# Performance work log

Measured on AMD Instinct MI355X. Metric: run time of the kernel, lower is better.

Reference implementation:

```python
import jax, jax.numpy as jnp
import numpy as np

B, S, E, H = 8, 1024, 1024, 16
D = E // H


def setup_inputs() -> dict:
    key = jax.random.key(0)
    ks = jax.random.split(key, 5)
    s = 1.0 / np.sqrt(E)
    return {
        "hidden_states": jax.random.normal(ks[0], (B, S, E), dtype=jnp.float32),
        "w_q": jax.random.normal(ks[1], (E, E), dtype=jnp.float32) * s,
        "w_k": jax.random.normal(ks[2], (E, E), dtype=jnp.float32) * s,
        "w_v": jax.random.normal(ks[3], (E, E), dtype=jnp.float32) * s,
        "w_out": jax.random.normal(ks[4], (E, E), dtype=jnp.float32) * s,
        "b_out": jnp.zeros((E,), dtype=jnp.float32),
    }


def reference(hidden_states, w_q, w_k, w_v, w_out, b_out):
    b, s = hidden_states.shape[0], hidden_states.shape[1]
    # Linear projections (weights stored as [in, out] = torch W^T)
    q = hidden_states @ w_q
    k = hidden_states @ w_k
    v = hidden_states @ w_v
    # Faithful to the original: raw reshape (B,S,E)->(B,H,S,D), NOT a head-split transpose
    q = q.reshape(b, H, s, D)
    k = k.reshape(b, H, s, D)
    v = v.reshape(b, H, s, D)
    # Scores scaled by embedding_size**-0.5 (original quirk, not head_dim**-0.5)
    scores = jnp.einsum("bhsd,bhtd->bhst", q, k) * (E ** -0.5)
    attn = jax.nn.softmax(scores, axis=-1)
    out = jnp.einsum("bhst,bhtd->bhsd", attn, v)  # [B,H,S,D]
    out = out.transpose(0, 2, 1, 3).reshape(b, s, E)  # [B,S,E]
    return out @ w_out + b_out
```

## Files before the change

### kernel.cpp

```cpp
#include <hip/hip_runtime.h>
#include <hip/hip_bf16.h>
#include <stdint.h>
#include <stddef.h>

static constexpr int Bb = 8, Ss = 1024, Ee = 1024, Hh = 16, Dd = 64;
static constexpr int Mm = Bb * Ss;

typedef __attribute__((ext_vector_type(8))) short frag8;
typedef __attribute__((ext_vector_type(4))) float fx4;
typedef __attribute__((ext_vector_type(4))) short s4v;

#define GP(p) ((const __attribute__((address_space(1))) void*)(p))
#define LP(p) ((__attribute__((address_space(3))) void*)(p))

static constexpr float QSC = 0.045084220027780106f;

__device__ inline short f2bf(float x) {
  union { float f; unsigned u; } c; c.f = x;
  unsigned u = c.u;
  unsigned r = (u + 0x7FFFu + ((u >> 16) & 1u)) >> 16;
  return (short)r;
}

__global__ __launch_bounds__(256) void cvt_kernel(const float* __restrict__ in,
                                                  short* __restrict__ out, int n4) {
  int i = blockIdx.x * 256 + threadIdx.x;
  if (i >= n4) return;
  float4 v = *((const float4*)in + i);
  union { short s[4]; uint2 u; } o;
  o.s[0] = f2bf(v.x); o.s[1] = f2bf(v.y); o.s[2] = f2bf(v.z); o.s[3] = f2bf(v.w);
  *(uint2*)(out + (size_t)i * 4) = o.u;
}

__global__ __launch_bounds__(256) void transpose_cvt4(const float* __restrict__ w0,
                                                      const float* __restrict__ w1,
                                                      const float* __restrict__ w2,
                                                      const float* __restrict__ w3,
                                                      short* __restrict__ WtBase) {
  __shared__ short tile[32][33];
  const int z = blockIdx.z;
  const float* W = z == 0 ? w0 : (z == 1 ? w1 : (z == 2 ? w2 : w3));
  short* Wt = WtBase + (size_t)z * 1024 * 1024;
  const int bx = blockIdx.x * 32;
  const int by = blockIdx.y * 32;
  const int tx = threadIdx.x & 31, ty = threadIdx.x >> 5;
  #pragma unroll
  for (int j = 0; j < 32; j += 8)
    tile[ty + j][tx] = f2bf(W[(size_t)(by + ty + j) * 1024 + bx + tx]);
  __syncthreads();
  #pragma unroll
  for (int j = 0; j < 32; j += 8)
    Wt[(size_t)(bx + ty + j) * 1024 + by + tx] = tile[tx][ty + j];
}

__global__ __launch_bounds__(256) void transpose_v(const short* __restrict__ V,
                                                   short* __restrict__ Vt) {
  __shared__ short tile[64][65];
  const int bh = blockIdx.y;
  const int s0 = blockIdx.x * 64;
  const short* Vb = V + (size_t)bh * 65536;
  short* Vtb = Vt + (size_t)bh * 65536;
  const int tx = threadIdx.x & 63, ty = threadIdx.x >> 6;
  #pragma unroll
  for (int j = 0; j < 64; j += 4)
    tile[ty + j][tx] = Vb[(size_t)(s0 + ty + j) * 64 + tx];
  __syncthreads();
  #pragma unroll
  for (int j = 0; j < 64; j += 4)
    Vtb[(size_t)(ty + j) * 1024 + s0 + tx] = tile[tx][ty + j];
}

__global__ __launch_bounds__(512, 2) void gemm_qkv_8ph(const short* __restrict__ A,
                                                       const short* __restrict__ Bt,
                                                       short* __restrict__ Cq,
                                                       short* __restrict__ Ck,
                                                       short* __restrict__ Cv) {
  __shared__ short As[2][16384];
  __shared__ short Bs[2][16384];
  const int t = threadIdx.x;
  const int w = t >> 6, lane = t & 63;
  const int fm = lane & 15, quad = lane >> 4;
  const int wm = w >> 1, wn = w & 1;
  const int wg = (blockIdx.x & 7) * 48 + (blockIdx.x >> 3);
  const int nt_i = wg % 12, mt_i = wg / 12;
  const int m0 = mt_i * 256, n0 = nt_i * 256;

  int goffA[4], goffB[4];
  #pragma unroll
  for (int i = 0; i < 4; ++i) {
    int c = i * 512 + t, row = c >> 3, col8 = (c & 7) ^ (row & 7);
    goffA[i] = row * 1024 + col8 * 8;
  }
  {
    int row32 = (t >> 3) & 31, hv = t >> 8, col8 = (t & 7) ^ (row32 & 7);
    #pragma unroll
    for (int j = 0; j < 4; ++j)
      goffB[j] = (hv * 128 + j * 32 + row32) * 1024 + col8 * 8;
  }
  const short* Ag = A + (size_t)m0 * 1024;
  const short* Bg = Bt + (size_t)n0 * 1024;

  fx4 acc[4][8];
  #pragma unroll
  for (int i = 0; i < 4; ++i)
    #pragma unroll
    for (int j = 0; j < 8; ++j) acc[i][j] = (fx4){0.f, 0.f, 0.f, 0.f};

  const int s0o = ((0 * 4 + quad) ^ (fm & 7)) * 8;
  const int s1o = ((1 * 4 + quad) ^ (fm & 7)) * 8;
  const int aBase = (wm * 64 + fm) * 64;
  const int bBase = wn * 2048 + fm * 64;

#define STG_A(i, koff, dstbuf) \
  __builtin_amdgcn_global_load_lds(GP(Ag + (koff) + goffA[i]), \
                                   LP((dstbuf) + ((i) * 512 + t) * 8), 16, 0, 0)
#define STG_B(j, koff, dstbuf) \
  __builtin_amdgcn_global_load_lds(GP(Bg + (koff) + goffB[j]), \
                                   LP((dstbuf) + ((j) * 512 + t) * 8), 16, 0, 0)
#define LOAD_B(p) \
  { const short* bp = Bb + (p) * 4096 + bBase; \
    bf[0][0] = *(const frag8*)(bp + s0o); \
    bf[0][1] = *(const frag8*)(bp + s1o); \
    bf[1][0] = *(const frag8*)(bp + 1024 + s0o); \
    bf[1][1] = *(const frag8*)(bp + 1024 + s1o); }
#define MFMA_PH(p) \
  __builtin_amdgcn_s_barrier(); \
  asm volatile("s_waitcnt lgkmcnt(0)" ::: "memory"); \
  __builtin_amdgcn_s_setprio(1); \
  _Pragma("unroll") \
  for (int mf = 0; mf < 4; ++mf) { \
    acc[mf][2*(p)]   = __builtin_amdgcn_mfma_f32_16x16x32_bf16(af[mf][0], bf[0][0], acc[mf][2*(p)],   0, 0, 0); \
    acc[mf][2*(p)]   = __builtin_amdgcn_mfma_f32_16x16x32_bf16(af[mf][1], bf[0][1], acc[mf][2*(p)],   0, 0, 0); \
    acc[mf][2*(p)+1] = __builtin_amdgcn_mfma_f32_16x16x32_bf16(af[mf][0], bf[1][0], acc[mf][2*(p)+1], 0, 0, 0); \
    acc[mf][2*(p)+1] = __builtin_amdgcn_mfma_f32_16x16x32_bf16(af[mf][1], bf[1][1], acc[mf][2*(p)+1], 0, 0, 0); \
  } \
  __builtin_amdgcn_s_setprio(0);

  #pragma unroll
  for (int i = 0; i < 4; ++i) STG_A(i, 0, &As[0][0]);
  #pragma unroll
  for (int j = 0; j < 4; ++j) STG_B(j, 0, &Bs[0][0]);
  asm volatile("s_waitcnt vmcnt(0)" ::: "memory");
  __builtin_amdgcn_s_barrier();

  for (int kt = 0; kt < 16; ++kt) {
    const short* Ab = As[kt & 1];
    const short* Bb = Bs[kt & 1];
    short* An = (short*)As[(kt & 1) ^ 1];
    short* Bn = (short*)Bs[(kt & 1) ^ 1];
    const int kn = (kt + 1) * 64;
    const bool pf = kt < 15;
    frag8 af[4][2], bf[2][2];

    #pragma unroll
    for (int mf = 0; mf < 4; ++mf) {
      const short* ap = Ab + aBase + mf * 1024;
      af[mf][0] = *(const frag8*)(ap + s0o);
      af[mf][1] = *(const frag8*)(ap + s1o);
    }
    LOAD_B(0);
    if (pf) {
      STG_A(0, kn, An); STG_A(1, kn, An); STG_A(2, kn, An); STG_A(3, kn, An);
      STG_B(0, kn, Bn); STG_B(1, kn, Bn); STG_B(2, kn, Bn); STG_B(3, kn, Bn);
    }
    MFMA_PH(0);
    __builtin_amdgcn_s_barrier();

    LOAD_B(1);
    MFMA_PH(1);
    __builtin_amdgcn_s_barrier();

    LOAD_B(2);
    MFMA_PH(2);
    __builtin_amdgcn_s_barrier();

    LOAD_B(3);
    MFMA_PH(3);
    if (pf) {
      asm volatile("s_waitcnt vmcnt(0)" ::: "memory");
      __builtin_amdgcn_s_barrier();
    }
  }
#undef STG_A
#undef STG_B
#undef LOAD_B
#undef MFMA_PH

  const int nb = n0 >> 10;
  short* dst = nb == 0 ? Cq : (nb == 1 ? Ck : Cv);
  const float scl = (nb == 0) ? QSC : 1.0f;
  const int nl0 = (n0 & 1023) + wn * 128;
  const int rbase = m0 + wm * 64 + quad * 4;
  #pragma unroll
  for (int mf = 0; mf < 4; ++mf)
    #pragma unroll
    for (int nf = 0; nf < 8; ++nf)
      #pragma unroll
      for (int r = 0; r < 4; ++r) {
        int row = rbase + mf * 16 + r;
        int col = nl0 + nf * 16 + fm;
        dst[(size_t)row * 1024 + col] = f2bf(acc[mf][nf][r] * scl);
      }
}

template <int MODE>
__global__ __launch_bounds__(256) void gemm_bt(const short* __restrict__ A,
                                               const short* __restrict__ Bt,
                                               void* __restrict__ C0,
                                               void* __restrict__ C1,
                                               void* __restrict__ C2,
                                               const float* __restrict__ bias,
                                               int M, int N, int K) {
  __shared__ short As[128 * 32];
  __shared__ short Bs[128 * 32];
  const int t = threadIdx.x;
  const int w = t >> 6, lane = t & 63;
  const int fm = lane & 15, quad = lane >> 4;
  const int m0 = blockIdx.y * 128, n0 = blockIdx.x * 128;
  const int wm = (w >> 1) * 64, wn = (w & 1) * 64;
  fx4 acc[4][4];
  #pragma unroll
  for (int i = 0; i < 4; ++i)
    #pragma unroll
    for (int j = 0; j < 4; ++j) acc[i][j] = (fx4){0.f, 0.f, 0.f, 0.f};

  for (int k0 = 0; k0 < K; k0 += 32) {
    #pragma unroll
    for (int i = 0; i < 2; ++i) {
      int chunk = i * 256 + t;
      int row = chunk >> 2, cc = chunk & 3;
      __builtin_amdgcn_global_load_lds(GP(A + (size_t)(m0 + row) * K + k0 + cc * 8),
                                       LP(As + chunk * 8), 16, 0, 0);
      __builtin_amdgcn_global_load_lds(GP(Bt + (size_t)(n0 + row) * K + k0 + cc * 8),
                                       LP(Bs + chunk * 8), 16, 0, 0);
    }
    __syncthreads();
    frag8 af[4], bfr[4];
    #pragma unroll
    for (int mt = 0; mt < 4; ++mt)
      af[mt] = *(const frag8*)(As + (wm + mt * 16 + fm) * 32 + quad * 8);
    #pragma unroll
    for (int nt = 0; nt < 4; ++nt)
      bfr[nt] = *(const frag8*)(Bs + (wn + nt * 16 + fm) * 32 + quad * 8);
    #pragma unroll
    for (int mt = 0; mt < 4; ++mt)
      #pragma unroll
      for (int nt = 0; nt < 4; ++nt)
        acc[mt][nt] = __builtin_amdgcn_mfma_f32_16x16x32_bf16(af[mt], bfr[nt], acc[mt][nt], 0, 0, 0);
    __syncthreads();
  }
  #pragma unroll
  for (int mt = 0; mt < 4; ++mt)
    #pragma unroll
    for (int nt = 0; nt < 4; ++nt)
      #pragma unroll
      for (int r = 0; r < 4; ++r) {
        int row = m0 + wm + mt * 16 + quad * 4 + r;
        int col = n0 + wn + nt * 16 + fm;
        ((float*)C0)[(size_t)row * N + col] = acc[mt][nt][r] + bias[col];
      }
}

__global__ __launch_bounds__(256, 2) void attn_kernel(const short* __restrict__ Q,
                                                      const short* __restrict__ K,
                                                      const short* __restrict__ Vt,
                                                      short* __restrict__ Ctx) {
  __shared__ short Ks[2][4096];
  __shared__ short Vs[2][4096];
  __shared__ short Plds[4 * 64 * 72];
  const int bh = blockIdx.x, qt = blockIdx.y;
  const int t = threadIdx.x;
  const int w = t >> 6, lane = t & 63;
  const int fm = lane & 15, quad = lane >> 4;
  const short* Qb = Q + (size_t)bh * 65536;
  const short* Kb = K + (size_t)bh * 65536;
  const short* Vb = Vt + (size_t)bh * 65536;
  const int q0 = qt * 256 + w * 64;
  short* myP = Plds + w * 4608;

  frag8 qb[4][2];
  #pragma unroll
  for (int g = 0; g < 4; ++g)
    #pragma unroll
    for (int h = 0; h < 2; ++h)
      qb[g][h] = *(const frag8*)(Qb + (size_t)(q0 + g * 16 + fm) * 64 + h * 32 + quad * 8);

  fx4 O[4][4];
  #pragma unroll
  for (int g = 0; g < 4; ++g)
    #pragma unroll
    for (int nt = 0; nt < 4; ++nt) O[g][nt] = (fx4){0.f, 0.f, 0.f, 0.f};
  float lp[4] = {0.f, 0.f, 0.f, 0.f};

  int koff[2], voff[2], loff[2];
  #pragma unroll
  for (int i = 0; i < 2; ++i) {
    int c = i * 256 + t;
    int cf = c & 15, cq = (c >> 4) & 3, ch = (c >> 6) & 1, cg = c >> 7;
    koff[i] = (cg * 16 + cf) * 64 + ch * 32 + cq * 8;
    voff[i] = (cg * 16 + cf) * 1024 + ch * 32 + cq * 8;
    loff[i] = c * 8;
  }

  #pragma unroll
  for (int i = 0; i < 2; ++i) {
    __builtin_amdgcn_global_load_lds(GP(Kb + koff[i]), LP(&Ks[0][0] + loff[i]), 16, 0, 0);
    __builtin_amdgcn_global_load_lds(GP(Vb + voff[i]), LP(&Vs[0][0] + loff[i]), 16, 0, 0);
  }
  __syncthreads();

  for (int c = 0; c < 16; ++c) {
    const int cur = c & 1;
    if (c < 15) {
      const int key0n = (c + 1) * 64;
      #pragma unroll
      for (int i = 0; i < 2; ++i) {
        __builtin_amdgcn_global_load_lds(GP(Kb + (size_t)key0n * 64 + koff[i]),
                                         LP(&Ks[cur ^ 1][0] + loff[i]), 16, 0, 0);
        __builtin_amdgcn_global_load_lds(GP(Vb + (size_t)key0n + voff[i]),
                                         LP(&Vs[cur ^ 1][0] + loff[i]), 16, 0, 0);
      }
    }
    const short* Kc = &Ks[cur][0];
    const short* Vc = &Vs[cur][0];

    #pragma unroll
    for (int s = 0; s < 4; ++s) {
      frag8 k0 = *(const frag8*)(Kc + (s * 2 + 0) * 512 + lane * 8);
      frag8 k1 = *(const frag8*)(Kc + (s * 2 + 1) * 512 + lane * 8);
      #pragma unroll
      for (int g = 0; g < 4; ++g) {
        fx4 z = (fx4){0.f, 0.f, 0.f, 0.f};
        z = __builtin_amdgcn_mfma_f32_16x16x32_bf16(k0, qb[g][0], z, 0, 0, 0);
        z = __builtin_amdgcn_mfma_f32_16x16x32_bf16(k1, qb[g][1], z, 0, 0, 0);
        s4v pv;
        #pragma unroll
        for (int r = 0; r < 4; ++r) {
          float p = __builtin_amdgcn_exp2f(z[r]);
          lp[g] += p;
          union { float f; unsigned u; } cv; cv.f = p;
          pv[r] = (short)(cv.u >> 16);
        }
        *(s4v*)(myP + (g * 16 + fm) * 72 + s * 16 + quad * 4) = pv;
      }
    }
    asm volatile("s_waitcnt lgkmcnt(0)" ::: "memory");
    #pragma unroll
    for (int h = 0; h < 2; ++h) {
      frag8 pf[4];
      #pragma unroll
      for (int g = 0; g < 4; ++g)
        pf[g] = *(const frag8*)(myP + (g * 16 + fm) * 72 + h * 32 + quad * 8);
      #pragma unroll
      for (int nt = 0; nt < 4; ++nt) {
        frag8 vf = *(const frag8*)(Vc + (nt * 2 + h) * 512 + lane * 8);
        #pragma unroll
        for (int g = 0; g < 4; ++g)
          O[g][nt] = __builtin_amdgcn_mfma_f32_16x16x32_bf16(pf[g], vf, O[g][nt], 0, 0, 0);
      }
    }
    __syncthreads();
  }

  float rl[4][4];
  #pragma unroll
  for (int g = 0; g < 4; ++g) {
    float v = lp[g];
    v += __shfl_xor(v, 16, 64);
    v += __shfl_xor(v, 32, 64);
    float inv = 1.f / v;
    #pragma unroll
    for (int r = 0; r < 4; ++r) rl[g][r] = __shfl(inv, quad * 4 + r, 16);
  }
  const int b = bh >> 4, h = bh & 15;
  #pragma unroll
  for (int g = 0; g < 4; ++g)
    #pragma unroll
    for (int nt = 0; nt < 4; ++nt)
      #pragma unroll
      for (int r = 0; r < 4; ++r) {
        int row = b * 1024 + q0 + g * 16 + quad * 4 + r;
        int col = h * 64 + nt * 16 + fm;
        Ctx[(size_t)row * 1024 + col] = f2bf(O[g][nt][r] * rl[g][r]);
      }
}

extern "C" void kernel_launch(void* const* d_in, const int* in_sizes, int n_in,
                              void* d_out, int out_size, void* d_ws, size_t ws_size,
                              hipStream_t stream) {
  const float* hs = (const float*)d_in[0];
  const float* wq = (const float*)d_in[1];
  const float* wk = (const float*)d_in[2];
  const float* wv = (const float*)d_in[3];
  const float* wo = (const float*)d_in[4];
  const float* bo = (const float*)d_in[5];
  float* out = (float*)d_out;

  char* wp = (char*)d_ws;
  const size_t MB16 = (size_t)Mm * Ee * 2;
  const size_t MB2  = (size_t)Ee * Ee * 2;
  short* Xb  = (short*)wp; wp += MB16;
  short* Wqt = (short*)wp; wp += MB2;
  short* Wkt = (short*)wp; wp += MB2;
  short* Wvt = (short*)wp; wp += MB2;
  short* Wot = (short*)wp; wp += MB2;
  short* Qb  = (short*)wp; wp += MB16;
  short* Kb  = (short*)wp; wp += MB16;
  short* Vb  = (short*)wp; wp += MB16;
  short* Vt  = (short*)wp; wp += MB16;
  short* Ctx = (short*)wp; wp += MB16;

  cvt_kernel<<<(Mm * Ee / 4 + 255) / 256, 256, 0, stream>>>(hs, Xb, Mm * Ee / 4);
  transpose_cvt4<<<dim3(32, 32, 4), 256, 0, stream>>>(wq, wk, wv, wo, Wqt);
  gemm_qkv_8ph<<<384, 512, 0, stream>>>(Xb, Wqt, Qb, Kb, Vb);
  transpose_v<<<dim3(16, 128), 256, 0, stream>>>(Vb, Vt);
  attn_kernel<<<dim3(128, 4), 256, 0, stream>>>(Qb, Kb, Vt, Ctx);
  gemm_bt<1><<<dim3(8, 64), 256, 0, stream>>>(Ctx, Wot, out, nullptr, nullptr, bo, Mm, Ee, Ee);
}
```

Measured before the change: 254.4 us.

## Shrink QKV GEMM tile to 128x256 with split-phase async staging

Halves the M tile of the fused QKV GEMM from 256 to 128 rows and rearranges the 8 waves as 2x4, with each wave computing 64x64. This doubles the grid to 768 blocks and halves the A-tile LDS footprint. The per-k-step schedule goes from four compute phases to two, and the next tile's global-to-LDS loads are split across them with partial vmcnt waits instead of a full drain. The intent is better occupancy and wave balance across CUs plus more overlap of loads with MFMA, at the cost of lower arithmetic intensity per block and more redundant B-tile traffic.

After: 251.0 us. No clear change (-1.3%).

```diff
diff --git a/kernel.cpp b/kernel.cpp
--- a/kernel.cpp
+++ b/kernel.cpp
@@ -75,41 +75,42 @@
                                                        short* __restrict__ Cq,
                                                        short* __restrict__ Ck,
                                                        short* __restrict__ Cv) {
-  __shared__ short As[2][16384];
+  __shared__ short As[2][8192];
   __shared__ short Bs[2][16384];
   const int t = threadIdx.x;
   const int w = t >> 6, lane = t & 63;
   const int fm = lane & 15, quad = lane >> 4;
-  const int wm = w >> 1, wn = w & 1;
-  const int wg = (blockIdx.x & 7) * 48 + (blockIdx.x >> 3);
+  const int wm = w >> 2, wn = w & 3;
+  const int wg = (blockIdx.x & 7) * 96 + (blockIdx.x >> 3);
   const int nt_i = wg % 12, mt_i = wg / 12;
-  const int m0 = mt_i * 256, n0 = nt_i * 256;
-
-  int goffA[4], goffB[4];
-  #pragma unroll
-  for (int i = 0; i < 4; ++i) {
+  const int m0 = mt_i * 128, n0 = nt_i * 256;
+
+  int goffA[2], goffB[4];
+  #pragma unroll
+  for (int i = 0; i < 2; ++i) {
     int c = i * 512 + t, row = c >> 3, col8 = (c & 7) ^ (row & 7);
     goffA[i] = row * 1024 + col8 * 8;
   }
-  {
-    int row32 = (t >> 3) & 31, hv = t >> 8, col8 = (t & 7) ^ (row32 & 7);
-    #pragma unroll
-    for (int j = 0; j < 4; ++j)
-      goffB[j] = (hv * 128 + j * 32 + row32) * 1024 + col8 * 8;
+  #pragma unroll
+  for (int j = 0; j < 4; ++j) {
+    int u = j >> 1, i = j & 1;
+    int c = i * 512 + t, r = c >> 3, col8 = (c & 7) ^ (r & 7);
+    int n = (r >> 5) * 64 + u * 32 + (r & 31);
+    goffB[j] = n * 1024 + col8 * 8;
   }
   const short* Ag = A + (size_t)m0 * 1024;
   const short* Bg = Bt + (size_t)n0 * 1024;
 
-  fx4 acc[4][8];
+  fx4 acc[4][4];
   #pragma unroll
   for (int i = 0; i < 4; ++i)
     #pragma unroll
-    for (int j = 0; j < 8; ++j) acc[i][j] = (fx4){0.f, 0.f, 0.f, 0.f};
-
-  const int s0o = ((0 * 4 + quad) ^ (fm & 7)) * 8;
-  const int s1o = ((1 * 4 + quad) ^ (fm & 7)) * 8;
+    for (int j = 0; j < 4; ++j) acc[i][j] = (fx4){0.f, 0.f, 0.f, 0.f};
+
+  const int s0o = (quad ^ (fm & 7)) * 8;
+  const int s1o = ((4 + quad) ^ (fm & 7)) * 8;
   const int aBase = (wm * 64 + fm) * 64;
-  const int bBase = wn * 2048 + fm * 64;
+  const int bBase = (wn * 32 + fm) * 64;
 
 #define STG_A(i, koff, dstbuf) \
   __builtin_amdgcn_global_load_lds(GP(Ag + (koff) + goffA[i]), \
@@ -118,7 +119,7 @@
   __builtin_amdgcn_global_load_lds(GP(Bg + (koff) + goffB[j]), \
                                    LP((dstbuf) + ((j) * 512 + t) * 8), 16, 0, 0)
 #define LOAD_B(p) \
-  { const short* bp = Bb + (p) * 4096 + bBase; \
+  { const short* bp = Bb + (p) * 8192 + bBase; \
     bf[0][0] = *(const frag8*)(bp + s0o); \
     bf[0][1] = *(const frag8*)(bp + s1o); \
     bf[1][0] = *(const frag8*)(bp + 1024 + s0o); \
@@ -136,11 +137,10 @@
   } \
   __builtin_amdgcn_s_setprio(0);
 
-  #pragma unroll
-  for (int i = 0; i < 4; ++i) STG_A(i, 0, &As[0][0]);
-  #pragma unroll
-  for (int j = 0; j < 4; ++j) STG_B(j, 0, &Bs[0][0]);
-  asm volatile("s_waitcnt vmcnt(0)" ::: "memory");
+  STG_A(0, 0, &As[0][0]); STG_A(1, 0, &As[0][0]);
+  STG_B(0, 0, &Bs[0][0]); STG_B(1, 0, &Bs[0][0]);
+  STG_B(2, 0, &Bs[0][0]); STG_B(3, 0, &Bs[0][0]);
+  asm volatile("s_waitcnt vmcnt(2)" ::: "memory");
   __builtin_amdgcn_s_barrier();
 
   for (int kt = 0; kt < 16; ++kt) {
@@ -159,25 +159,17 @@
       af[mf][1] = *(const frag8*)(ap + s1o);
     }
     LOAD_B(0);
+    if (pf) { STG_A(0, kn, An); STG_A(1, kn, An); STG_B(0, kn, Bn); STG_B(1, kn, Bn); }
+    MFMA_PH(0);
+    if (pf) asm volatile("s_waitcnt vmcnt(4)" ::: "memory");
+    else    asm volatile("s_waitcnt vmcnt(0)" ::: "memory");
+    __builtin_amdgcn_s_barrier();
+
+    LOAD_B(1);
+    if (pf) { STG_B(2, kn, Bn); STG_B(3, kn, Bn); }
+    MFMA_PH(1);
     if (pf) {
-      STG_A(0, kn, An); STG_A(1, kn, An); STG_A(2, kn, An); STG_A(3, kn, An);
-      STG_B(0, kn, Bn); STG_B(1, kn, Bn); STG_B(2, kn, Bn); STG_B(3, kn, Bn);
-    }
-    MFMA_PH(0);
-    __builtin_amdgcn_s_barrier();
-
-    LOAD_B(1);
-    MFMA_PH(1);
-    __builtin_amdgcn_s_barrier();
-
-    LOAD_B(2);
-    MFMA_PH(2);
-    __builtin_amdgcn_s_barrier();
-
-    LOAD_B(3);
-    MFMA_PH(3);
-    if (pf) {
-      asm volatile("s_waitcnt vmcnt(0)" ::: "memory");
+      asm volatile("s_waitcnt vmcnt(2)" ::: "memory");
       __builtin_amdgcn_s_barrier();
     }
   }
@@ -189,12 +181,12 @@
   const int nb = n0 >> 10;
   short* dst = nb == 0 ? Cq : (nb == 1 ? Ck : Cv);
   const float scl = (nb == 0) ? QSC : 1.0f;
-  const int nl0 = (n0 & 1023) + wn * 128;
+  const int nl0 = (n0 & 1023) + wn * 64;
   const int rbase = m0 + wm * 64 + quad * 4;
   #pragma unroll
   for (int mf = 0; mf < 4; ++mf)
     #pragma unroll
-    for (int nf = 0; nf < 8; ++nf)
+    for (int nf = 0; nf < 4; ++nf)
       #pragma unroll
       for (int r = 0; r < 4; ++r) {
         int row = rbase + mf * 16 + r;
@@ -412,7 +404,7 @@
 
   cvt_kernel<<<(Mm * Ee / 4 + 255) / 256, 256, 0, stream>>>(hs, Xb, Mm * Ee / 4);
   transpose_cvt4<<<dim3(32, 32, 4), 256, 0, stream>>>(wq, wk, wv, wo, Wqt);
-  gemm_qkv_8ph<<<384, 512, 0, stream>>>(Xb, Wqt, Qb, Kb, Vb);
+  gemm_qkv_8ph<<<768, 512, 0, stream>>>(Xb, Wqt, Qb, Kb, Vb);
   transpose_v<<<dim3(16, 128), 256, 0, stream>>>(Vb, Vt);
   attn_kernel<<<dim3(128, 4), 256, 0, stream>>>(Qb, Kb, Vt, Ctx);
   gemm_bt<1><<<dim3(8, 64), 256, 0, stream>>>(Ctx, Wot, out, nullptr, nullptr, bo, Mm, Ee, Ee);
```
